# Kernel optimization log

Hardware: AMD Instinct MI355X
Metric: run time of the kernel (lower is better)

Reference implementation:

```python
import jax, jax.numpy as jnp
import numpy as np

N_DRUG, N_GENE = 20000, 40000
D_DRUG, D_GENE = 128, 64
HID, EMB = 64, 32
E_DD, E_DG, E_GG = 1500000, 1000000, 1500000


def setup_inputs() -> dict:
    key = jax.random.key(0)
    ks = iter(jax.random.split(key, 32))

    def nrm(shape, scale=0.05):
        return jax.random.normal(next(ks), shape, dtype=jnp.float32) * scale

    def idx(n, e):
        return jax.random.randint(next(ks), (e,), 0, n, dtype=jnp.int32)

    return dict(
        feat_drug=nrm((N_DRUG, D_DRUG), 1.0),
        feat_gene=nrm((N_GENE, D_GENE), 1.0),
        dd_src=idx(N_DRUG, E_DD), dd_dst=idx(N_DRUG, E_DD),
        dg_src=idx(N_DRUG, E_DG), dg_dst=idx(N_GENE, E_DG),
        gg_src=idx(N_GENE, E_GG), gg_dst=idx(N_GENE, E_GG),
        neg_src=idx(N_DRUG, E_DD), neg_dst=idx(N_DRUG, E_DD),
        W1_dd=nrm((D_DRUG, HID)), W1_dg=nrm((D_DRUG, HID)), W1_gg=nrm((D_GENE, HID)),
        W1_self_drug=nrm((D_DRUG, HID)), W1_self_gene=nrm((D_GENE, HID)),
        b1=jnp.zeros((HID,), jnp.float32),
        W2_dd=nrm((HID, EMB)), W2_dg=nrm((HID, EMB)), W2_gg=nrm((HID, EMB)),
        W2_self_drug=nrm((HID, EMB)), W2_self_gene=nrm((HID, EMB)),
        b2=jnp.zeros((EMB,), jnp.float32),
        w_rel=nrm((EMB,), 1.0),
    )


def _mean_agg(msg_nodes, src, dst, n_dst):
    # transform-then-gather: msg_nodes is [n_src, out]; gather per edge, scatter-sum to dst,
    # divide by dst in-degree (DGL GraphConv norm='right').
    m = jax.ops.segment_sum(msg_nodes[src], dst, num_segments=n_dst)
    deg = jax.ops.segment_sum(jnp.ones(dst.shape, msg_nodes.dtype), dst, num_segments=n_dst)
    return m / jnp.clip(deg, 1.0)[:, None]


def _rel_layer(hd, hg, edges, Wdd, Wdg, Wgg, Wsd, Wsg, b, act):
    dd_src, dd_dst, dg_src, dg_dst, gg_src, gg_dst = edges
    # per-relation linear transform on src nodes, then mean aggregation to dst;
    # sum across relations sharing the same dst node type (HeteroGraphConv aggregate='sum')
    agg_d = _mean_agg(hd @ Wdd, dd_src, dd_dst, hd.shape[0])
    agg_g = (_mean_agg(hd @ Wdg, dg_src, dg_dst, hg.shape[0])
             + _mean_agg(hg @ Wgg, gg_src, gg_dst, hg.shape[0]))
    out_d = agg_d + hd @ Wsd + b  # self-loop + bias
    out_g = agg_g + hg @ Wsg + b
    if act:
        out_d, out_g = jax.nn.relu(out_d), jax.nn.relu(out_g)
    return out_d, out_g


def reference(feat_drug, feat_gene, dd_src, dd_dst, dg_src, dg_dst, gg_src, gg_dst,
              neg_src, neg_dst, W1_dd, W1_dg, W1_gg, W1_self_drug, W1_self_gene, b1,
              W2_dd, W2_dg, W2_gg, W2_self_drug, W2_self_gene, b2, w_rel):
    edges = (dd_src, dd_dst, dg_src, dg_dst, gg_src, gg_dst)
    h_d, h_g = _rel_layer(feat_drug, feat_gene, edges,
                          W1_dd, W1_dg, W1_gg, W1_self_drug, W1_self_gene, b1, True)
    h_d, h_g = _rel_layer(h_d, h_g, edges,
                          W2_dd, W2_dg, W2_gg, W2_self_drug, W2_self_gene, b2, False)
    # per-edge-type diagonal-bilinear dot-product scorer, etype='dd' (drug-drug)
    pos = jnp.sum(h_d[dd_src] * w_rel * h_d[dd_dst], axis=-1)
    neg = jnp.sum(h_d[neg_src] * w_rel * h_d[neg_dst], axis=-1)
    return pos, neg
```

## Files before the change

### kernel.cpp

```cpp
#include <hip/hip_runtime.h>


#define NPART 8

__device__ inline float bf2f(unsigned short b) {
    union { float f; unsigned u; } c; c.u = (unsigned)b << 16; return c.f;
}
__device__ inline unsigned short f2bf(float x) {
    union { float f; unsigned u; } c; c.f = x;
    unsigned r = c.u + 0x7FFF + ((c.u >> 16) & 1);
    return (unsigned short)(r >> 16);
}

template<int KIN>
__global__ __launch_bounds__(256) void gemm_reg_kernel(const float* __restrict__ A,
                                                       const float* __restrict__ W,
                                                       unsigned short* __restrict__ out,
                                                       int M) {
    const int lane = threadIdx.x & 63;
    const int gwave = blockIdx.x * (blockDim.x >> 6) + (threadIdx.x >> 6);
    const int nwave = gridDim.x * (blockDim.x >> 6);
    float w[KIN];
#pragma unroll
    for (int k = 0; k < KIN; ++k) w[k] = W[k * 64 + lane];
    for (int m0 = gwave * 2; m0 < M; m0 += nwave * 2) {
        const int mu = __builtin_amdgcn_readfirstlane(m0);
        const float* a0 = A + (size_t)mu * KIN;
        const float* a1 = a0 + KIN;
        const bool two = (mu + 1) < M;
        float acc0 = 0.0f, acc1 = 0.0f;
#pragma unroll
        for (int k = 0; k < KIN; ++k) {
            const float av0 = a0[k];
            const float av1 = two ? a1[k] : 0.0f;
            acc0 = fmaf(av0, w[k], acc0);
            acc1 = fmaf(av1, w[k], acc1);
        }
        out[(size_t)mu * 64 + lane] = f2bf(acc0);
        if (two) out[(size_t)(mu + 1) * 64 + lane] = f2bf(acc1);
    }
}

__global__ __launch_bounds__(256) void gemm2_reg_kernel(const float* __restrict__ A,
                                                        const float* __restrict__ Wa,
                                                        const float* __restrict__ Wb,
                                                        unsigned short* __restrict__ out_a,
                                                        unsigned short* __restrict__ out_b,
                                                        int M) {
    const int lane = threadIdx.x & 63;
    const int col = lane & 31;
    const float* Wm = (lane < 32) ? Wa : Wb;
    unsigned short* om = (lane < 32) ? out_a : out_b;
    const int gwave = blockIdx.x * (blockDim.x >> 6) + (threadIdx.x >> 6);
    const int nwave = gridDim.x * (blockDim.x >> 6);
    float w[64];
#pragma unroll
    for (int k = 0; k < 64; ++k) w[k] = Wm[k * 32 + col];
    for (int m0 = gwave * 2; m0 < M; m0 += nwave * 2) {
        const int mu = __builtin_amdgcn_readfirstlane(m0);
        const float* a0 = A + (size_t)mu * 64;
        const float* a1 = a0 + 64;
        const bool two = (mu + 1) < M;
        float acc0 = 0.0f, acc1 = 0.0f;
#pragma unroll
        for (int k = 0; k < 64; ++k) {
            const float av0 = a0[k];
            const float av1 = two ? a1[k] : 0.0f;
            acc0 = fmaf(av0, w[k], acc0);
            acc1 = fmaf(av1, w[k], acc1);
        }
        om[(size_t)mu * 32 + col] = f2bf(acc0);
        if (two) om[(size_t)(mu + 1) * 32 + col] = f2bf(acc1);
    }
}

__global__ __launch_bounds__(256) void degree8_kernel(const int* __restrict__ dst,
                                                      int* __restrict__ deg8,
                                                      int E, int chunk, int N) {
    const int p = blockIdx.x & (NPART - 1);
    const int lo = p * chunk;
    const int hi = min(lo + chunk, E);
    int* __restrict__ deg = deg8 + (size_t)p * N;
    const int bip = blockIdx.x >> 3;
    const int stride = (gridDim.x >> 3) * 256;
    for (int e = lo + bip * 256 + threadIdx.x; e < hi; e += stride) {
        const int d = __builtin_nontemporal_load(dst + e);
        atomicAdd(&deg[d], 1);
    }
}

__global__ __launch_bounds__(1024) void scan8_kernel(const int* __restrict__ deg8,
                                                     int* __restrict__ off8,
                                                     int* __restrict__ cursor8,
                                                     int N, int chunk) {
    const int p = blockIdx.x;
    const int base = p * chunk;
    const int* __restrict__ deg = deg8 + (size_t)p * N;
    int* __restrict__ off = off8 + (size_t)p * N;
    int* __restrict__ cur = cursor8 + (size_t)p * N;
    __shared__ int part[1024];
    const int t = threadIdx.x;
    const int per = (N + 1023) / 1024;
    const int beg = t * per;
    const int end = min(beg + per, N);
    int s = 0;
    for (int i = beg; i < end; ++i) s += deg[i];
    part[t] = s;
    __syncthreads();
    for (int d = 1; d < 1024; d <<= 1) {
        int v = (t >= d) ? part[t - d] : 0;
        __syncthreads();
        part[t] += v;
        __syncthreads();
    }
    int run = base + ((t == 0) ? 0 : part[t - 1]);
    for (int i = beg; i < end; ++i) { off[i] = run; cur[i] = run; run += deg[i]; }
}

__global__ __launch_bounds__(256) void fill8_kernel(const int* __restrict__ src,
                                                    const int* __restrict__ dst,
                                                    int* __restrict__ cursor8,
                                                    unsigned short* __restrict__ csr_src,
                                                    int E, int chunk, int N) {
    const int p = blockIdx.x & (NPART - 1);
    const int lo = p * chunk;
    const int hi = min(lo + chunk, E);
    int* __restrict__ cursor = cursor8 + (size_t)p * N;
    const int bip = blockIdx.x >> 3;
    const int stride = (gridDim.x >> 3) * 256;
    for (int e = lo + bip * 256 + threadIdx.x; e < hi; e += stride) {
        const int d = __builtin_nontemporal_load(dst + e);
        const int s = __builtin_nontemporal_load(src + e);
        const int pos = atomicAdd(&cursor[d], 1);
        csr_src[pos] = (unsigned short)s;
    }
}

template<int W, bool RELU, bool OBF>
__global__ __launch_bounds__(256) void gather_combine_kernel(
        const unsigned short* __restrict__ msg,
        const unsigned short* __restrict__ csr_src,
        const int* __restrict__ off8, const int* __restrict__ end8,
        const unsigned short* __restrict__ selfb, const float* __restrict__ b,
        void* __restrict__ out_, int N) {
    const int GRP = 256 / W;
    const int g = threadIdx.x / W;
    const int lane = threadIdx.x % W;
    const float bk = b[lane];
    for (int n = blockIdx.x * GRP + g; n < N; n += gridDim.x * GRP) {
        float acc = 0.0f;
        int cnt = 0;
        for (int p = 0; p < NPART; ++p) {
            const int beg = off8[(size_t)p * N + n];
            const int end = end8[(size_t)p * N + n];
            cnt += end - beg;
            int i = beg;
            for (; i + 4 <= end; i += 4) {
                const int s0 = __builtin_nontemporal_load(csr_src + i);
                const int s1 = __builtin_nontemporal_load(csr_src + i + 1);
                const int s2 = __builtin_nontemporal_load(csr_src + i + 2);
                const int s3 = __builtin_nontemporal_load(csr_src + i + 3);
                const float v0 = bf2f(msg[(size_t)s0 * W + lane]);
                const float v1 = bf2f(msg[(size_t)s1 * W + lane]);
                const float v2 = bf2f(msg[(size_t)s2 * W + lane]);
                const float v3 = bf2f(msg[(size_t)s3 * W + lane]);
                acc += (v0 + v1) + (v2 + v3);
            }
            for (; i < end; ++i)
                acc += bf2f(msg[(size_t)__builtin_nontemporal_load(csr_src + i) * W + lane]);
        }
        const float d = (cnt > 0) ? (float)cnt : 1.0f;
        float v = acc / d + bf2f(__builtin_nontemporal_load(selfb + (size_t)n * W + lane)) + bk;
        if (RELU) v = fmaxf(v, 0.0f);
        if (OBF) ((unsigned short*)out_)[(size_t)n * W + lane] = f2bf(v);
        else     ((float*)out_)[(size_t)n * W + lane] = v;
    }
}

__global__ __launch_bounds__(256) void score2_kernel(const unsigned short* __restrict__ h,
                                                     const int* __restrict__ sA,
                                                     const int* __restrict__ dA,
                                                     const int* __restrict__ sB,
                                                     const int* __restrict__ dB,
                                                     const float* __restrict__ wrel,
                                                     float* __restrict__ outA,
                                                     float* __restrict__ outB,
                                                     int EA, int EB) {
    const int lj = threadIdx.x & 7;
    const size_t grp = ((size_t)blockIdx.x * blockDim.x + threadIdx.x) >> 3;
    const size_t ngrp = ((size_t)gridDim.x * blockDim.x) >> 3;
    const float4 w = *(const float4*)(wrel + lj * 4);
    const size_t total = (size_t)EA + (size_t)EB;
    for (size_t e = grp; e < total; e += ngrp) {
        int s, d; float* o;
        if (e < (size_t)EA) {
            s = __builtin_nontemporal_load(sA + e);
            d = __builtin_nontemporal_load(dA + e);
            o = outA + e;
        } else {
            const size_t e2 = e - EA;
            s = __builtin_nontemporal_load(sB + e2);
            d = __builtin_nontemporal_load(dB + e2);
            o = outB + e2;
        }
        const ushort4 hs = *(const ushort4*)(h + (size_t)s * 32 + lj * 4);
        const ushort4 hd = *(const ushort4*)(h + (size_t)d * 32 + lj * 4);
        float p = bf2f(hs.x) * w.x * bf2f(hd.x) + bf2f(hs.y) * w.y * bf2f(hd.y) +
                  bf2f(hs.z) * w.z * bf2f(hd.z) + bf2f(hs.w) * w.w * bf2f(hd.w);
        p += __shfl_xor(p, 1, 64);
        p += __shfl_xor(p, 2, 64);
        p += __shfl_xor(p, 4, 64);
        if (lj == 0) __builtin_nontemporal_store(p, o);
    }
}

extern "C" void kernel_launch(void* const* d_in, const int* in_sizes, int n_in,
                              void* d_out, int out_size, void* d_ws, size_t ws_size,
                              hipStream_t stream) {
    const float* feat_drug    = (const float*)d_in[0];
    const int*   dd_src       = (const int*)d_in[2];
    const int*   dd_dst       = (const int*)d_in[3];
    const int*   neg_src      = (const int*)d_in[8];
    const int*   neg_dst      = (const int*)d_in[9];
    const float* W1_dd        = (const float*)d_in[10];
    const float* W1_self_drug = (const float*)d_in[13];
    const float* b1           = (const float*)d_in[15];
    const float* W2_dd        = (const float*)d_in[16];
    const float* W2_self_drug = (const float*)d_in[19];
    const float* b2           = (const float*)d_in[21];
    const float* w_rel        = (const float*)d_in[22];

    const int N  = in_sizes[0] / 128;
    const int E  = in_sizes[2];
    const int EN = in_sizes[8];
    const int CHUNK = (E + NPART - 1) / NPART;
    const int M8 = NPART * N;

    char* ws = (char*)d_ws;
    int*            deg8    = (int*)ws;            ws += (size_t)M8 * 4;
    int*            off8    = (int*)ws;            ws += (size_t)M8 * 4;
    int*            cursor8 = (int*)ws;            ws += (size_t)M8 * 4;
    unsigned short* csr16   = (unsigned short*)ws; ws += (size_t)E * 2;
    ws = (char*)(((size_t)ws + 3) & ~(size_t)3);
    unsigned short* msg1    = (unsigned short*)ws; ws += (size_t)N * 64 * 2;
    unsigned short* self1   = (unsigned short*)ws; ws += (size_t)N * 64 * 2;
    unsigned short* msg2    = (unsigned short*)ws; ws += (size_t)N * 32 * 2;
    unsigned short* self2   = (unsigned short*)ws; ws += (size_t)N * 32 * 2;
    unsigned short* h2      = (unsigned short*)ws; ws += (size_t)N * 32 * 2;
    ws = (char*)(((size_t)ws + 3) & ~(size_t)3);
    float*          h1      = (float*)ws;          ws += (size_t)N * 64 * 4;

    float* pos = (float*)d_out;
    float* neg = pos + E;

    hipMemsetAsync(deg8, 0, (size_t)M8 * sizeof(int), stream);

    degree8_kernel<<<2048, 256, 0, stream>>>(dd_dst, deg8, E, CHUNK, N);
    scan8_kernel<<<NPART, 1024, 0, stream>>>(deg8, off8, cursor8, N, CHUNK);
    fill8_kernel<<<2048, 256, 0, stream>>>(dd_src, dd_dst, cursor8, csr16, E, CHUNK, N);

    gemm_reg_kernel<128><<<512, 256, 0, stream>>>(feat_drug, W1_dd, msg1, N);
    gemm_reg_kernel<128><<<512, 256, 0, stream>>>(feat_drug, W1_self_drug, self1, N);
    gather_combine_kernel<64, true, false><<<(N + 3) / 4, 256, 0, stream>>>(
        msg1, csr16, off8, cursor8, self1, b1, h1, N);

    gemm2_reg_kernel<<<512, 256, 0, stream>>>(h1, W2_dd, W2_self_drug, msg2, self2, N);
    gather_combine_kernel<32, false, true><<<(N + 7) / 8, 256, 0, stream>>>(
        msg2, csr16, off8, cursor8, self2, b2, h2, N);

    score2_kernel<<<4096, 256, 0, stream>>>(h2, dd_src, dd_dst, neg_src, neg_dst,
                                            w_rel, pos, neg, E, EN);
}
```

Measured before the change: 444.6 us.

## Gather edges in parallel per wavefront with paired bf16 loads; widen score loads

The gather kernels now give each node a full wavefront. Lanes are split into feature pairs and edge slots, so several edges are read at once with 32-bit loads, and the partial sums are reduced with cross-lane shuffles. This replaces the old scheme where each node's W threads walked its edges one after another. The scorer now uses 4 lanes per edge with 16-byte loads instead of 8 lanes with 8-byte loads, and the workspace buffers are aligned to 16 bytes to allow this. The trade-offs are extra shuffle and reduction work per node and idle slots on nodes of low degree.

```diff
diff --git a/kernel.cpp b/kernel.cpp
--- a/kernel.cpp
+++ b/kernel.cpp
@@ -11,6 +11,8 @@
     unsigned r = c.u + 0x7FFF + ((c.u >> 16) & 1);
     return (unsigned short)(r >> 16);
 }
+__device__ inline float bflo(unsigned u) { return bf2f((unsigned short)(u & 0xFFFF)); }
+__device__ inline float bfhi(unsigned u) { return bf2f((unsigned short)(u >> 16)); }
 
 template<int KIN>
 __global__ __launch_bounds__(256) void gemm_reg_kernel(const float* __restrict__ A,
@@ -137,43 +139,53 @@
 }
 
 template<int W, bool RELU, bool OBF>
-__global__ __launch_bounds__(256) void gather_combine_kernel(
+__global__ __launch_bounds__(256) void gather2_kernel(
         const unsigned short* __restrict__ msg,
-        const unsigned short* __restrict__ csr_src,
+        const unsigned short* __restrict__ csr,
         const int* __restrict__ off8, const int* __restrict__ end8,
         const unsigned short* __restrict__ selfb, const float* __restrict__ b,
         void* __restrict__ out_, int N) {
-    const int GRP = 256 / W;
-    const int g = threadIdx.x / W;
-    const int lane = threadIdx.x % W;
-    const float bk = b[lane];
-    for (int n = blockIdx.x * GRP + g; n < N; n += gridDim.x * GRP) {
-        float acc = 0.0f;
+    constexpr int PAIRS = W / 2;
+    constexpr int SLOTS = 64 / PAIRS;
+    const int lane = threadIdx.x & 63;
+    const int fp   = lane & (PAIRS - 1);
+    const int slot = lane / PAIRS;
+    const int wid  = (blockIdx.x * blockDim.x + threadIdx.x) >> 6;
+    const int nw   = (gridDim.x * blockDim.x) >> 6;
+    const float bk0 = b[2 * fp], bk1 = b[2 * fp + 1];
+    for (int n = wid; n < N; n += nw) {
+        float a0 = 0.0f, a1 = 0.0f;
         int cnt = 0;
         for (int p = 0; p < NPART; ++p) {
             const int beg = off8[(size_t)p * N + n];
             const int end = end8[(size_t)p * N + n];
             cnt += end - beg;
-            int i = beg;
-            for (; i + 4 <= end; i += 4) {
-                const int s0 = __builtin_nontemporal_load(csr_src + i);
-                const int s1 = __builtin_nontemporal_load(csr_src + i + 1);
-                const int s2 = __builtin_nontemporal_load(csr_src + i + 2);
-                const int s3 = __builtin_nontemporal_load(csr_src + i + 3);
-                const float v0 = bf2f(msg[(size_t)s0 * W + lane]);
-                const float v1 = bf2f(msg[(size_t)s1 * W + lane]);
-                const float v2 = bf2f(msg[(size_t)s2 * W + lane]);
-                const float v3 = bf2f(msg[(size_t)s3 * W + lane]);
-                acc += (v0 + v1) + (v2 + v3);
+            for (int i = beg; i < end; i += SLOTS) {
+                const int e = i + slot;
+                const bool valid = e < end;
+                const int s = valid ? (int)csr[e] : 0;
+                const unsigned u = *(const unsigned*)(msg + (size_t)s * W + fp * 2);
+                if (valid) { a0 += bflo(u); a1 += bfhi(u); }
             }
-            for (; i < end; ++i)
-                acc += bf2f(msg[(size_t)__builtin_nontemporal_load(csr_src + i) * W + lane]);
-        }
-        const float d = (cnt > 0) ? (float)cnt : 1.0f;
-        float v = acc / d + bf2f(__builtin_nontemporal_load(selfb + (size_t)n * W + lane)) + bk;
-        if (RELU) v = fmaxf(v, 0.0f);
-        if (OBF) ((unsigned short*)out_)[(size_t)n * W + lane] = f2bf(v);
-        else     ((float*)out_)[(size_t)n * W + lane] = v;
+        }
+#pragma unroll
+        for (int d = PAIRS; d < 64; d <<= 1) {
+            a0 += __shfl_xor(a0, d, 64);
+            a1 += __shfl_xor(a1, d, 64);
+        }
+        if (slot == 0) {
+            const float dn = (cnt > 0) ? (float)cnt : 1.0f;
+            const unsigned sb = *(const unsigned*)(selfb + (size_t)n * W + fp * 2);
+            float v0 = a0 / dn + bflo(sb) + bk0;
+            float v1 = a1 / dn + bfhi(sb) + bk1;
+            if (RELU) { v0 = fmaxf(v0, 0.0f); v1 = fmaxf(v1, 0.0f); }
+            if (OBF) {
+                ((unsigned*)out_)[(size_t)n * PAIRS + fp] =
+                    (unsigned)f2bf(v0) | ((unsigned)f2bf(v1) << 16);
+            } else {
+                ((float2*)out_)[(size_t)n * PAIRS + fp] = make_float2(v0, v1);
+            }
+        }
     }
 }
 
@@ -186,10 +198,12 @@
                                                      float* __restrict__ outA,
                                                      float* __restrict__ outB,
                                                      int EA, int EB) {
-    const int lj = threadIdx.x & 7;
-    const size_t grp = ((size_t)blockIdx.x * blockDim.x + threadIdx.x) >> 3;
-    const size_t ngrp = ((size_t)gridDim.x * blockDim.x) >> 3;
-    const float4 w = *(const float4*)(wrel + lj * 4);
+    const int lj = threadIdx.x & 3;
+    const size_t grp = ((size_t)blockIdx.x * blockDim.x + threadIdx.x) >> 2;
+    const size_t ngrp = ((size_t)gridDim.x * blockDim.x) >> 2;
+    float w[8];
+#pragma unroll
+    for (int j = 0; j < 8; ++j) w[j] = wrel[lj * 8 + j];
     const size_t total = (size_t)EA + (size_t)EB;
     for (size_t e = grp; e < total; e += ngrp) {
         int s, d; float* o;
@@ -203,13 +217,14 @@
             d = __builtin_nontemporal_load(dB + e2);
             o = outB + e2;
         }
-        const ushort4 hs = *(const ushort4*)(h + (size_t)s * 32 + lj * 4);
-        const ushort4 hd = *(const ushort4*)(h + (size_t)d * 32 + lj * 4);
-        float p = bf2f(hs.x) * w.x * bf2f(hd.x) + bf2f(hs.y) * w.y * bf2f(hd.y) +
-                  bf2f(hs.z) * w.z * bf2f(hd.z) + bf2f(hs.w) * w.w * bf2f(hd.w);
+        const uint4 us = *(const uint4*)(h + (size_t)s * 32 + lj * 8);
+        const uint4 ud = *(const uint4*)(h + (size_t)d * 32 + lj * 8);
+        float p = bflo(us.x) * w[0] * bflo(ud.x) + bfhi(us.x) * w[1] * bfhi(ud.x)
+                + bflo(us.y) * w[2] * bflo(ud.y) + bfhi(us.y) * w[3] * bfhi(ud.y)
+                + bflo(us.z) * w[4] * bflo(ud.z) + bfhi(us.z) * w[5] * bfhi(ud.z)
+                + bflo(us.w) * w[6] * bflo(ud.w) + bfhi(us.w) * w[7] * bfhi(ud.w);
         p += __shfl_xor(p, 1, 64);
         p += __shfl_xor(p, 2, 64);
-        p += __shfl_xor(p, 4, 64);
         if (lj == 0) __builtin_nontemporal_store(p, o);
     }
 }
@@ -241,13 +256,13 @@
     int*            off8    = (int*)ws;            ws += (size_t)M8 * 4;
     int*            cursor8 = (int*)ws;            ws += (size_t)M8 * 4;
     unsigned short* csr16   = (unsigned short*)ws; ws += (size_t)E * 2;
-    ws = (char*)(((size_t)ws + 3) & ~(size_t)3);
+    ws = (char*)(((size_t)ws + 15) & ~(size_t)15);
     unsigned short* msg1    = (unsigned short*)ws; ws += (size_t)N * 64 * 2;
     unsigned short* self1   = (unsigned short*)ws; ws += (size_t)N * 64 * 2;
     unsigned short* msg2    = (unsigned short*)ws; ws += (size_t)N * 32 * 2;
     unsigned short* self2   = (unsigned short*)ws; ws += (size_t)N * 32 * 2;
     unsigned short* h2      = (unsigned short*)ws; ws += (size_t)N * 32 * 2;
-    ws = (char*)(((size_t)ws + 3) & ~(size_t)3);
+    ws = (char*)(((size_t)ws + 15) & ~(size_t)15);
     float*          h1      = (float*)ws;          ws += (size_t)N * 64 * 4;
 
     float* pos = (float*)d_out;
@@ -261,11 +276,11 @@
 
     gemm_reg_kernel<128><<<512, 256, 0, stream>>>(feat_drug, W1_dd, msg1, N);
     gemm_reg_kernel<128><<<512, 256, 0, stream>>>(feat_drug, W1_self_drug, self1, N);
-    gather_combine_kernel<64, true, false><<<(N + 3) / 4, 256, 0, stream>>>(
+    gather2_kernel<64, true, false><<<(N + 3) / 4, 256, 0, stream>>>(
         msg1, csr16, off8, cursor8, self1, b1, h1, N);
 
     gemm2_reg_kernel<<<512, 256, 0, stream>>>(h1, W2_dd, W2_self_drug, msg2, self2, N);
-    gather_combine_kernel<32, false, true><<<(N + 7) / 8, 256, 0, stream>>>(
+    gather2_kernel<32, false, true><<<(N + 3) / 4, 256, 0, stream>>>(
         msg2, csr16, off8, cursor8, self2, b2, h2, N);
 
     score2_kernel<<<4096, 256, 0, stream>>>(h2, dd_src, dd_dst, neg_src, neg_dst,
```

Result: faster. 409.9 us (-7.8%).
